# Optimization experiments

Measured on AMD Instinct MI355X. Metric: run time of the kernel, lower is better.

Reference implementation:

```python
import jax, jax.numpy as jnp
import numpy as np

N_NODES, BATCH, VOCAB, HID, OUT = 2047, 128, 32, 128, 128


def setup_inputs() -> dict:
    key = jax.random.key(0)
    ks = jax.random.split(key, 18)
    w = 0.05  # small init scale (xavier-ish for these sizes)
    rn = lambda k, s, sc=w: jax.random.normal(k, s, dtype=jnp.float32) * sc
    return {
        "targets": jax.random.normal(ks[0], (N_NODES, BATCH, VOCAB), dtype=jnp.float32),
        "masks": jnp.ones((N_NODES, BATCH), dtype=jnp.float32),
        "wir_w": rn(ks[1], (HID, VOCAB)), "wir_b": rn(ks[2], (HID,)),
        "whr_w": rn(ks[3], (HID, 2 * HID)), "whr_b": rn(ks[4], (HID,)),
        "wiz_w": rn(ks[5], (HID, VOCAB)), "wiz_b": rn(ks[6], (HID,)),
        "whz_w": rn(ks[7], (HID, 2 * HID)), "whz_b": rn(ks[8], (HID,)),
        "win_w": rn(ks[9], (HID, VOCAB)), "win_b": rn(ks[10], (HID,)),
        "whn_w": rn(ks[11], (HID, 2 * HID)), "whn_b": rn(ks[12], (HID,)),
        "mu_w": rn(ks[13], (OUT, HID)), "mu_b": rn(ks[14], (OUT,)),
        "lv_w": rn(ks[15], (OUT, HID)), "lv_b": rn(ks[16], (OUT,)),
    }


def _encode(targets, masks, wir_w, wir_b, whr_w, whr_b, wiz_w, wiz_b,
            whz_w, whz_b, win_w, win_b, whn_w, whn_b):
    # Complete binary tree in heap layout: level d occupies nodes [2^d-1, 2^(d+1)-1).
    # Bottom-up level sweep == the original node-by-node recursion, but each
    # level's GRU221 cells are batched into one fused GEMM group.
    Nn, B, V = targets.shape
    H = wir_w.shape[0]
    D = int(np.log2(Nn + 1))  # static at trace time
    h_prev = None  # hidden states of the level below, [2^(d+1)*B, H]
    for d in range(D - 1, -1, -1):
        n = 1 << d
        start = n - 1
        x = targets[start:start + n].reshape(n * B, V)
        m = masks[start:start + n].reshape(n * B, 1)
        if h_prev is None:  # leaves: zero children
            h1 = jnp.zeros((n * B, H), dtype=targets.dtype)
            h2 = h1
        else:
            hp = h_prev.reshape(2 * n, B, H)
            h1 = hp[0::2].reshape(n * B, H)  # left children (heap idx 2i+1)
            h2 = hp[1::2].reshape(n * B, H)  # right children (heap idx 2i+2)
        h = jnp.concatenate([h1, h2], axis=1)  # [nB, 2H]
        r = jax.nn.sigmoid(x @ wir_w.T + wir_b + h @ whr_w.T + whr_b)
        z = jax.nn.sigmoid(x @ wiz_w.T + wiz_b + h @ whz_w.T + whz_b)
        c = jnp.tanh(x @ win_w.T + win_b + r * (h @ whn_w.T + whn_b))
        h_out = (1 - z) * c + z * 0.5 * h1 + z * 0.5 * h2
        h_prev = h_out * m
    return h_prev  # root hidden, [B, H]


def reference(targets, masks, wir_w, wir_b, whr_w, whr_b, wiz_w, wiz_b,
              whz_w, whz_b, win_w, win_b, whn_w, whn_b,
              mu_w, mu_b, lv_w, lv_b):
    root = _encode(targets, masks, wir_w, wir_b, whr_w, whr_b,
                   wiz_w, wiz_b, whz_w, whz_b, win_w, win_b, whn_w, whn_b)
    mu = root @ mu_w.T + mu_b
    logvar = root @ lv_w.T + lv_b
    return mu, logvar
```

## Files before the change

kernel.cpp:

```cpp
#include <hip/hip_runtime.h>
#include <hip/hip_bf16.h>
#include <math.h>

#define B 128
#define V 32
#define H 128
#define LDH 264
#define NT 512

typedef __attribute__((ext_vector_type(8))) short bf16x8;
typedef __attribute__((ext_vector_type(4))) float f32x4;

__device__ inline f32x4 mfma_wx(bf16x8 wf, bf16x8 xf, f32x4 c) {
    return __builtin_amdgcn_mfma_f32_16x16x32_bf16(wf, xf, c, 0, 0, 0);
}
__device__ inline unsigned short f2bf(float f) {
    __hip_bfloat16 h = __float2bfloat16(f);
    return __builtin_bit_cast(unsigned short, h);
}
__device__ inline float bf2f(unsigned short u) {
    unsigned int x = ((unsigned int)u) << 16;
    return __builtin_bit_cast(float, x);
}
__device__ inline float sig_pre(float y)  { return __builtin_amdgcn_rcpf(1.f + __builtin_amdgcn_exp2f(y)); }
__device__ inline float tanh_pre(float y) { return 1.f - 2.f * __builtin_amdgcn_rcpf(__builtin_amdgcn_exp2f(y) + 1.f); }
__device__ inline bf16x8 load_xfrag(const float* p) {
    float4 a = *(const float4*)p;
    float4 b = *(const float4*)(p + 4);
    bf16x8 r;
    r[0] = (short)f2bf(a.x); r[1] = (short)f2bf(a.y);
    r[2] = (short)f2bf(a.z); r[3] = (short)f2bf(a.w);
    r[4] = (short)f2bf(b.x); r[5] = (short)f2bf(b.y);
    r[6] = (short)f2bf(b.z); r[7] = (short)f2bf(b.w);
    return r;
}
__device__ inline uint2 pack4(float a, float b, float c, float d) {
    uint2 r;
    r.x = (unsigned int)f2bf(a) | ((unsigned int)f2bf(b) << 16);
    r.y = (unsigned int)f2bf(c) | ((unsigned int)f2bf(d) << 16);
    return r;
}

__global__ void prep_pack(const float* __restrict__ wir_w, const float* __restrict__ whr_w,
                          const float* __restrict__ wiz_w, const float* __restrict__ whz_w,
                          const float* __restrict__ win_w, const float* __restrict__ whn_w,
                          const float* __restrict__ wir_b, const float* __restrict__ whr_b,
                          const float* __restrict__ wiz_b, const float* __restrict__ whz_b,
                          const float* __restrict__ win_b, const float* __restrict__ whn_b,
                          const float* __restrict__ mu_w, const float* __restrict__ mu_b,
                          const float* __restrict__ lv_w, const float* __restrict__ lv_b,
                          unsigned short* __restrict__ wFrag, unsigned short* __restrict__ pFrag,
                          float* __restrict__ bias)
{
    int idx = blockIdx.x * blockDim.x + threadIdx.x;
    if (idx < 13824) {
        int lane = idx & 63;
        int ctks = idx >> 6;
        int ct = ctks % 24;
        int ks = ctks / 24;
        int g = ct >> 3;
        int t = ct & 7;
        int u = t * 16 + (lane & 15);
        const float scl = (g == 2) ? 2.88539008f : -1.44269504f;
        const float* wi = (g == 0) ? wir_w : (g == 1) ? wiz_w : win_w;
        const float* wh = (g == 0) ? whr_w : (g == 1) ? whz_w : whn_w;
        unsigned short v[8] __attribute__((aligned(16)));
        #pragma unroll
        for (int i = 0; i < 8; ++i) {
            float f;
            if (ks == 0) { int k = 8 * (lane >> 4) + i; f = wi[u * V + k]; }
            else         { int k = (ks - 1) * 32 + 8 * (lane >> 4) + i; f = wh[u * 256 + k]; }
            v[i] = f2bf(f * scl);
        }
        *(int4*)(wFrag + (size_t)idx * 8) = *(const int4*)v;
    } else if (idx < 13824 + 4096) {
        int pidx = idx - 13824;
        int lane = pidx & 63;
        int rest = pidx >> 6;
        int ct2 = rest & 15;
        int ks = rest >> 4;
        int sel = ct2 >> 3, tl = ct2 & 7;
        int u = tl * 16 + (lane & 15);
        const float* wsrc = sel ? lv_w : mu_w;
        unsigned short v[8] __attribute__((aligned(16)));
        #pragma unroll
        for (int i = 0; i < 8; ++i) {
            int k = ks * 32 + 8 * (lane >> 4) + i;
            v[i] = f2bf(wsrc[u * H + k]);
        }
        *(int4*)(pFrag + (size_t)pidx * 8) = *(const int4*)v;
    }
    if (idx < 6 * H) {
        int s = idx / H, u = idx % H;
        float val;
        if (s == 0)      val = (wir_b[u] + whr_b[u]) * -1.44269504f;
        else if (s == 1) val = (wiz_b[u] + whz_b[u]) * -1.44269504f;
        else if (s == 2) val = win_b[u] * 2.88539008f;
        else if (s == 3) val = whn_b[u] * 2.88539008f;
        else if (s == 4) val = mu_b[u];
        else             val = lv_b[u];
        bias[idx] = val;
    }
}

template <typename EMIT>
__device__ __forceinline__ void gru32_body(
    const unsigned short* __restrict__ wFrag, const float* __restrict__ bias,
    bf16x8 x0, bf16x8 x1, float m0, float m1,
    const unsigned short* __restrict__ hin,
    int lane, int w, EMIT emit)
{
    const int l15 = lane & 15;
    const int lg = lane >> 4;
    const int u0 = w * 16 + lg * 4;

    f32x4 acc_r[2], acc_z[2], acc_i[2], acc_h[2];
    {
        f32x4 b0 = *(const f32x4*)(bias + u0);
        f32x4 b1 = *(const f32x4*)(bias + 128 + u0);
        f32x4 b2 = *(const f32x4*)(bias + 256 + u0);
        f32x4 b3 = *(const f32x4*)(bias + 384 + u0);
        acc_r[0] = b0; acc_r[1] = b0;
        acc_z[0] = b1; acc_z[1] = b1;
        acc_i[0] = b2; acc_i[1] = b2;
        acc_h[0] = b3; acc_h[1] = b3;
    }
    {
        bf16x8 wr_ = *(const bf16x8*)(wFrag + ((size_t)(w) * 64 + lane) * 8);
        bf16x8 wz_ = *(const bf16x8*)(wFrag + ((size_t)(8 + w) * 64 + lane) * 8);
        bf16x8 wn_ = *(const bf16x8*)(wFrag + ((size_t)(16 + w) * 64 + lane) * 8);
        acc_r[0] = mfma_wx(wr_, x0, acc_r[0]);
        acc_r[1] = mfma_wx(wr_, x1, acc_r[1]);
        acc_z[0] = mfma_wx(wz_, x0, acc_z[0]);
        acc_z[1] = mfma_wx(wz_, x1, acc_z[1]);
        acc_i[0] = mfma_wx(wn_, x0, acc_i[0]);
        acc_i[1] = mfma_wx(wn_, x1, acc_i[1]);
    }
    #pragma unroll 2
    for (int ks = 1; ks <= 8; ++ks) {
        bf16x8 a0 = *(const bf16x8*)(&hin[l15 * LDH + (ks - 1) * 32 + 8 * lg]);
        bf16x8 a1 = *(const bf16x8*)(&hin[(16 + l15) * LDH + (ks - 1) * 32 + 8 * lg]);
        size_t fb = (size_t)ks * 24 * 64;
        bf16x8 wr_ = *(const bf16x8*)(wFrag + (fb + (size_t)(w) * 64 + lane) * 8);
        bf16x8 wz_ = *(const bf16x8*)(wFrag + (fb + (size_t)(8 + w) * 64 + lane) * 8);
        bf16x8 wn_ = *(const bf16x8*)(wFrag + (fb + (size_t)(16 + w) * 64 + lane) * 8);
        acc_r[0] = mfma_wx(wr_, a0, acc_r[0]);
        acc_r[1] = mfma_wx(wr_, a1, acc_r[1]);
        acc_z[0] = mfma_wx(wz_, a0, acc_z[0]);
        acc_z[1] = mfma_wx(wz_, a1, acc_z[1]);
        acc_h[0] = mfma_wx(wn_, a0, acc_h[0]);
        acc_h[1] = mfma_wx(wn_, a1, acc_h[1]);
    }
    #pragma unroll
    for (int rt = 0; rt < 2; ++rt) {
        float m = rt ? m1 : m0;
        int hrow = rt * 16 + l15;
        ushort4 h1v = *(const ushort4*)(&hin[hrow * LDH + u0]);
        ushort4 h2v = *(const ushort4*)(&hin[hrow * LDH + 128 + u0]);
        const unsigned short* h1p = (const unsigned short*)&h1v;
        const unsigned short* h2p = (const unsigned short*)&h2v;
        float ho[4];
        #pragma unroll
        for (int reg = 0; reg < 4; ++reg) {
            float rg = sig_pre(acc_r[rt][reg]);
            float zg = sig_pre(acc_z[rt][reg]);
            float cg = tanh_pre(acc_i[rt][reg] + rg * acc_h[rt][reg]);
            float hm = 0.5f * bf2f(h1p[reg]) + 0.5f * bf2f(h2p[reg]);
            ho[reg] = (cg + zg * (hm - cg)) * m;
        }
        emit(rt, u0, pack4(ho[0], ho[1], ho[2], ho[3]));
    }
}

__device__ __forceinline__ void load_wreg(
    const unsigned short* __restrict__ wFrag, int lane, int w,
    bf16x8 (&wr)[9], bf16x8 (&wz)[9], bf16x8 (&wn)[9])
{
    #pragma unroll
    for (int ks = 0; ks < 9; ++ks) {
        size_t fb = (size_t)ks * 24 * 64;
        wr[ks] = *(const bf16x8*)(wFrag + (fb + (size_t)(w) * 64 + lane) * 8);
        wz[ks] = *(const bf16x8*)(wFrag + (fb + (size_t)(8 + w) * 64 + lane) * 8);
        wn[ks] = *(const bf16x8*)(wFrag + (fb + (size_t)(16 + w) * 64 + lane) * 8);
    }
}

template <typename EMIT>
__device__ __forceinline__ void gru32_ws(
    const bf16x8 (&wr)[9], const bf16x8 (&wz)[9], const bf16x8 (&wn)[9],
    const float* __restrict__ bias,
    bf16x8 x0, bf16x8 x1, float m0, float m1,
    const unsigned short* __restrict__ hin,
    int lane, int w, EMIT emit)
{
    const int l15 = lane & 15;
    const int lg = lane >> 4;
    const int u0 = w * 16 + lg * 4;

    f32x4 acc_r[2], acc_z[2], acc_i[2], acc_h[2];
    {
        f32x4 b0 = *(const f32x4*)(bias + u0);
        f32x4 b1 = *(const f32x4*)(bias + 128 + u0);
        f32x4 b2 = *(const f32x4*)(bias + 256 + u0);
        f32x4 b3 = *(const f32x4*)(bias + 384 + u0);
        acc_r[0] = b0; acc_r[1] = b0;
        acc_z[0] = b1; acc_z[1] = b1;
        acc_i[0] = b2; acc_i[1] = b2;
        acc_h[0] = b3; acc_h[1] = b3;
    }
    acc_r[0] = mfma_wx(wr[0], x0, acc_r[0]);
    acc_r[1] = mfma_wx(wr[0], x1, acc_r[1]);
    acc_z[0] = mfma_wx(wz[0], x0, acc_z[0]);
    acc_z[1] = mfma_wx(wz[0], x1, acc_z[1]);
    acc_i[0] = mfma_wx(wn[0], x0, acc_i[0]);
    acc_i[1] = mfma_wx(wn[0], x1, acc_i[1]);
    #pragma unroll
    for (int ks = 1; ks <= 8; ++ks) {
        bf16x8 a0 = *(const bf16x8*)(&hin[l15 * LDH + (ks - 1) * 32 + 8 * lg]);
        bf16x8 a1 = *(const bf16x8*)(&hin[(16 + l15) * LDH + (ks - 1) * 32 + 8 * lg]);
        acc_r[0] = mfma_wx(wr[ks], a0, acc_r[0]);
        acc_r[1] = mfma_wx(wr[ks], a1, acc_r[1]);
        acc_z[0] = mfma_wx(wz[ks], a0, acc_z[0]);
        acc_z[1] = mfma_wx(wz[ks], a1, acc_z[1]);
        acc_h[0] = mfma_wx(wn[ks], a0, acc_h[0]);
        acc_h[1] = mfma_wx(wn[ks], a1, acc_h[1]);
    }
    #pragma unroll
    for (int rt = 0; rt < 2; ++rt) {
        float m = rt ? m1 : m0;
        int hrow = rt * 16 + l15;
        ushort4 h1v = *(const ushort4*)(&hin[hrow * LDH + u0]);
        ushort4 h2v = *(const ushort4*)(&hin[hrow * LDH + 128 + u0]);
        const unsigned short* h1p = (const unsigned short*)&h1v;
        const unsigned short* h2p = (const unsigned short*)&h2v;
        float ho[4];
        #pragma unroll
        for (int reg = 0; reg < 4; ++reg) {
            float rg = sig_pre(acc_r[rt][reg]);
            float zg = sig_pre(acc_z[rt][reg]);
            float cg = tanh_pre(acc_i[rt][reg] + rg * acc_h[rt][reg]);
            float hm = 0.5f * bf2f(h1p[reg]) + 0.5f * bf2f(h2p[reg]);
            ho[reg] = (cg + zg * (hm - cg)) * m;
        }
        emit(rt, u0, pack4(ho[0], ho[1], ho[2], ho[3]));
    }
}

__global__ __launch_bounds__(NT, 4) void subtree8_kernel(
    const float* __restrict__ targets, const float* __restrict__ masks,
    unsigned short* __restrict__ lvl8,
    const unsigned short* __restrict__ wFrag, const float* __restrict__ bias)
{
    __shared__ __attribute__((aligned(16))) unsigned short h_lds[32 * LDH];
    __shared__ __attribute__((aligned(16))) unsigned short h2_lds[32 * LDH];

    const int tid = threadIdx.x;
    const int lane = tid & 63;
    const int w = tid >> 6;
    const int l15 = lane & 15;
    const int lg = lane >> 4;
    const int u0 = w * 16 + lg * 4;
    const int n = blockIdx.x >> 2;
    const int q = blockIdx.x & 3;

    for (int half = 0; half < 2; ++half) {
        const int j = 2 * n + half;
        const size_t r9 = (size_t)(511 + j) * B + (size_t)q * 32;

        #pragma unroll
        for (int c = 0; c < 2; ++c) {
            const size_t crow = (size_t)(1023 + 2 * j + c) * B + (size_t)q * 32;
            bf16x8 xf0 = load_xfrag(targets + (crow + l15) * V + 8 * lg);
            bf16x8 xf1 = load_xfrag(targets + (crow + 16 + l15) * V + 8 * lg);
            float m0 = masks[crow + l15];
            float m1 = masks[crow + 16 + l15];
            f32x4 ar[2], az[2], an[2], bh;
            {
                f32x4 b0 = *(const f32x4*)(bias + u0);
                f32x4 b1 = *(const f32x4*)(bias + 128 + u0);
                f32x4 b2 = *(const f32x4*)(bias + 256 + u0);
                bh       = *(const f32x4*)(bias + 384 + u0);
                ar[0] = b0; ar[1] = b0;
                az[0] = b1; az[1] = b1;
                an[0] = b2; an[1] = b2;
            }
            {
                bf16x8 wr_ = *(const bf16x8*)(wFrag + ((size_t)(w) * 64 + lane) * 8);
                bf16x8 wz_ = *(const bf16x8*)(wFrag + ((size_t)(8 + w) * 64 + lane) * 8);
                bf16x8 wn_ = *(const bf16x8*)(wFrag + ((size_t)(16 + w) * 64 + lane) * 8);
                ar[0] = mfma_wx(wr_, xf0, ar[0]);
                ar[1] = mfma_wx(wr_, xf1, ar[1]);
                az[0] = mfma_wx(wz_, xf0, az[0]);
                az[1] = mfma_wx(wz_, xf1, az[1]);
                an[0] = mfma_wx(wn_, xf0, an[0]);
                an[1] = mfma_wx(wn_, xf1, an[1]);
            }
            #pragma unroll
            for (int rt = 0; rt < 2; ++rt) {
                float m = rt ? m1 : m0;
                int row = rt * 16 + l15;
                float ho[4];
                #pragma unroll
                for (int reg = 0; reg < 4; ++reg) {
                    float rg = sig_pre(ar[rt][reg]);
                    float zg = sig_pre(az[rt][reg]);
                    float cg = tanh_pre(an[rt][reg] + rg * bh[reg]);
                    ho[reg] = (cg - zg * cg) * m;
                }
                *(uint2*)(&h_lds[row * LDH + c * 128 + u0]) = pack4(ho[0], ho[1], ho[2], ho[3]);
            }
        }
        __syncthreads();

        {
            bf16x8 x9_0 = load_xfrag(targets + (r9 + l15) * V + 8 * lg);
            bf16x8 x9_1 = load_xfrag(targets + (r9 + 16 + l15) * V + 8 * lg);
            float m0 = masks[r9 + l15];
            float m1 = masks[r9 + 16 + l15];
            gru32_body(wFrag, bias, x9_0, x9_1, m0, m1, h_lds, lane, w,
                [&](int rt, int uu, uint2 pk) {
                    int row = rt * 16 + l15;
                    *(uint2*)(&h2_lds[row * LDH + half * 128 + uu]) = pk;
                });
        }
        __syncthreads();
    }

    {
        const size_t r8 = (size_t)(255 + n) * B + (size_t)q * 32;
        bf16x8 x8_0 = load_xfrag(targets + (r8 + l15) * V + 8 * lg);
        bf16x8 x8_1 = load_xfrag(targets + (r8 + 16 + l15) * V + 8 * lg);
        float m0 = masks[r8 + l15];
        float m1 = masks[r8 + 16 + l15];
        gru32_body(wFrag, bias, x8_0, x8_1, m0, m1, h2_lds, lane, w,
            [&](int rt, int uu, uint2 pk) {
                int row = rt * 16 + l15;
                *(uint2*)(lvl8 + ((size_t)n * B + (size_t)q * 32 + row) * H + uu) = pk;
            });
    }
}

__global__ __launch_bounds__(NT, 2) void tail4_kernel(
    const float* __restrict__ targets, const float* __restrict__ masks,
    const unsigned short* __restrict__ prev,
    unsigned short* __restrict__ outg,
    int s3, int s2, int s1, int s0,
    const unsigned short* __restrict__ wFrag, const float* __restrict__ bias,
    int do_proj, const unsigned short* __restrict__ pFrag, float* __restrict__ proj_out)
{
    __shared__ __attribute__((aligned(16))) unsigned short hc[32 * LDH];
    __shared__ __attribute__((aligned(16))) unsigned short h6[2 * 32 * LDH];
    __shared__ __attribute__((aligned(16))) unsigned short h5[32 * LDH];
    __shared__ __attribute__((aligned(16))) unsigned short h4[16 * LDH];

    const int tid = threadIdx.x;
    const int lane = tid & 63;
    const int w = tid >> 6;
    const int l15 = lane & 15;
    const int lg = lane >> 4;
    const int u0 = w * 16 + lg * 4;
    const int pr = blockIdx.x >> 3;
    const int c8 = blockIdx.x & 7;

    bf16x8 wr[9], wz[9], wn[9];
    load_wreg(wFrag, lane, w, wr, wz, wn);

    for (int s = 0; s < 4; ++s) {
        const int l1 = 4 * pr + s;
        #pragma unroll
        for (int t = 0; t < 2; ++t) {
            int task = t * NT + tid;
            int row = task >> 5;
            int ck = task & 31;
            int g = 4 * l1 + 2 * (row >> 4) + (ck >> 4);
            int4 v = *(const int4*)(prev + (((size_t)g) * B + (size_t)c8 * 16 + (row & 15)) * H + (ck & 15) * 8);
            *(int4*)(&hc[row * LDH + ck * 8]) = v;
        }
        size_t xr0 = ((size_t)(s3 + 2 * l1)) * B + (size_t)c8 * 16 + l15;
        size_t xr1 = ((size_t)(s3 + 2 * l1 + 1)) * B + (size_t)c8 * 16 + l15;
        bf16x8 xc0 = load_xfrag(targets + xr0 * V + 8 * lg);
        bf16x8 xc1 = load_xfrag(targets + xr1 * V + 8 * lg);
        float m0 = masks[xr0];
        float m1 = masks[xr1];
        __syncthreads();
        unsigned short* hout = h6 + (size_t)(s >> 1) * 32 * LDH;
        int rowbase = 16 * (s & 1);
        gru32_ws(wr, wz, wn, bias, xc0, xc1, m0, m1, hc, lane, w,
            [&](int rt, int uu, uint2 pk) {
                *(uint2*)(&hout[(rowbase + l15) * LDH + rt * 128 + uu]) = pk;
            });
        __syncthreads();
    }

    for (int k = 0; k < 2; ++k) {
        int n1 = 4 * pr + 2 * k;
        size_t xr0 = ((size_t)(s2 + n1)) * B + (size_t)c8 * 16 + l15;
        size_t xr1 = ((size_t)(s2 + n1 + 1)) * B + (size_t)c8 * 16 + l15;
        bf16x8 xc0 = load_xfrag(targets + xr0 * V + 8 * lg);
        bf16x8 xc1 = load_xfrag(targets + xr1 * V + 8 * lg);
        float m0 = masks[xr0];
        float m1 = masks[xr1];
        const unsigned short* hin = h6 + (size_t)k * 32 * LDH;
        int rowbase = 16 * k;
        gru32_ws(wr, wz, wn, bias, xc0, xc1, m0, m1, hin, lane, w,
            [&](int rt, int uu, uint2 pk) {
                *(uint2*)(&h5[(rowbase + l15) * LDH + rt * 128 + uu]) = pk;
            });
    }
    __syncthreads();

    {
        size_t xr0 = ((size_t)(s1 + 2 * pr)) * B + (size_t)c8 * 16 + l15;
        size_t xr1 = ((size_t)(s1 + 2 * pr + 1)) * B + (size_t)c8 * 16 + l15;
        bf16x8 xc0 = load_xfrag(targets + xr0 * V + 8 * lg);
        bf16x8 xc1 = load_xfrag(targets + xr1 * V + 8 * lg);
        float m0 = masks[xr0];
        float m1 = masks[xr1];
        gru32_ws(wr, wz, wn, bias, xc0, xc1, m0, m1, h5, lane, w,
            [&](int rt, int uu, uint2 pk) {
                *(uint2*)(&h4[l15 * LDH + rt * 128 + uu]) = pk;
            });
    }
    __syncthreads();

    {
        size_t xrp = ((size_t)(s0 + pr)) * B + (size_t)c8 * 16 + l15;
        bf16x8 xp = load_xfrag(targets + xrp * V + 8 * lg);
        float m = masks[xrp];
        f32x4 acc_r = *(const f32x4*)(bias + u0);
        f32x4 acc_z = *(const f32x4*)(bias + 128 + u0);
        f32x4 acc_i = *(const f32x4*)(bias + 256 + u0);
        f32x4 acc_h = *(const f32x4*)(bias + 384 + u0);
        acc_r = mfma_wx(wr[0], xp, acc_r);
        acc_z = mfma_wx(wz[0], xp, acc_z);
        acc_i = mfma_wx(wn[0], xp, acc_i);
        #pragma unroll
        for (int ks = 1; ks <= 8; ++ks) {
            bf16x8 a = *(const bf16x8*)(&h4[l15 * LDH + (ks - 1) * 32 + 8 * lg]);
            acc_r = mfma_wx(wr[ks], a, acc_r);
            acc_z = mfma_wx(wz[ks], a, acc_z);
            acc_h = mfma_wx(wn[ks], a, acc_h);
        }
        ushort4 h1v = *(const ushort4*)(&h4[l15 * LDH + u0]);
        ushort4 h2v = *(const ushort4*)(&h4[l15 * LDH + 128 + u0]);
        const unsigned short* h1p = (const unsigned short*)&h1v;
        const unsigned short* h2p = (const unsigned short*)&h2v;
        float ho[4];
        #pragma unroll
        for (int reg = 0; reg < 4; ++reg) {
            float rg = sig_pre(acc_r[reg]);
            float zg = sig_pre(acc_z[reg]);
            float cg = tanh_pre(acc_i[reg] + rg * acc_h[reg]);
            float hm = 0.5f * bf2f(h1p[reg]) + 0.5f * bf2f(h2p[reg]);
            ho[reg] = (cg + zg * (hm - cg)) * m;
        }
        uint2 pk = pack4(ho[0], ho[1], ho[2], ho[3]);
        if (outg)
            *(uint2*)(outg + ((size_t)pr * B + (size_t)c8 * 16 + l15) * H + u0) = pk;
        if (do_proj)
            *(uint2*)(&hc[l15 * LDH + u0]) = pk;
    }

    if (do_proj) {
        __syncthreads();
        f32x4 pa[2];
        #pragma unroll
        for (int jj = 0; jj < 2; ++jj) {
            int ct2 = 2 * w + jj;
            int sel = ct2 >> 3, tl = ct2 & 7;
            pa[jj] = *(const f32x4*)(bias + 512 + sel * 128 + tl * 16 + lg * 4);
        }
        #pragma unroll
        for (int ks = 0; ks < 4; ++ks) {
            bf16x8 a = *(const bf16x8*)(&hc[l15 * LDH + ks * 32 + 8 * lg]);
            #pragma unroll
            for (int jj = 0; jj < 2; ++jj) {
                bf16x8 f = *(const bf16x8*)(pFrag + (((size_t)ks * 16 + 2 * w + jj) * 64 + lane) * 8);
                pa[jj] = mfma_wx(f, a, pa[jj]);
            }
        }
        #pragma unroll
        for (int jj = 0; jj < 2; ++jj) {
            int ct2 = 2 * w + jj;
            int sel = ct2 >> 3, tl = ct2 & 7;
            int up = tl * 16 + lg * 4;
            int row = c8 * 16 + l15;
            *(f32x4*)(proj_out + ((size_t)sel * B + row) * H + up) = pa[jj];
        }
    }
}

extern "C" void kernel_launch(void* const* d_in, const int* in_sizes, int n_in,
                              void* d_out, int out_size, void* d_ws, size_t ws_size,
                              hipStream_t stream)
{
    const float* targets = (const float*)d_in[0];
    const float* masks   = (const float*)d_in[1];
    const float* wir_w = (const float*)d_in[2];  const float* wir_b = (const float*)d_in[3];
    const float* whr_w = (const float*)d_in[4];  const float* whr_b = (const float*)d_in[5];
    const float* wiz_w = (const float*)d_in[6];  const float* wiz_b = (const float*)d_in[7];
    const float* whz_w = (const float*)d_in[8];  const float* whz_b = (const float*)d_in[9];
    const float* win_w = (const float*)d_in[10]; const float* win_b = (const float*)d_in[11];
    const float* whn_w = (const float*)d_in[12]; const float* whn_b = (const float*)d_in[13];
    const float* mu_w  = (const float*)d_in[14]; const float* mu_b  = (const float*)d_in[15];
    const float* lv_w  = (const float*)d_in[16]; const float* lv_b  = (const float*)d_in[17];

    unsigned short* ws16 = (unsigned short*)d_ws;
    unsigned short* lvl8 = ws16;
    unsigned short* lvl4 = lvl8 + (size_t)256 * B * H;
    unsigned short* wFrag = lvl4 + (size_t)16 * B * H;
    unsigned short* pFrag = wFrag + 110592;
    float*          biasw = (float*)(pFrag + 32768);

    prep_pack<<<70, 256, 0, stream>>>(
        wir_w, whr_w, wiz_w, whz_w, win_w, whn_w,
        wir_b, whr_b, wiz_b, whz_b, win_b, whn_b,
        mu_w, mu_b, lv_w, lv_b, wFrag, pFrag, biasw);

    subtree8_kernel<<<1024, NT, 0, stream>>>(targets, masks, lvl8, wFrag, biasw);

    tail4_kernel<<<128, NT, 0, stream>>>(
        targets, masks, lvl8, lvl4, 127, 63, 31, 15,
        wFrag, biasw, 0, nullptr, nullptr);

    tail4_kernel<<<8, NT, 0, stream>>>(
        targets, masks, lvl4, nullptr, 7, 3, 1, 0,
        wFrag, biasw, 1, pFrag, (float*)d_out);
}
```

Baseline: 110.2 us.

## Prefetch next-stage inputs and double-buffer child states to overlap loads with compute

In subtree8_kernel the loop over the two halves is unrolled by hand, and the global loads of targets for the second half and for level 8 are issued before the barrier and the compute of the prior stage. In tail4_kernel the staging buffer for child hidden states is double-buffered (hcA/hcB), so the next step's child states and targets are fetched from global memory while the current GRU step runs. This is meant to hide global load latency behind MFMA work and drop one barrier per step. In exchange it raises register pressure, and tail4's launch bounds drop to one block per SM to make room, which may cost occupancy.

```diff
diff --git a/kernel.cpp b/kernel.cpp
--- a/kernel.cpp
+++ b/kernel.cpp
@@ -24,15 +24,19 @@
 }
 __device__ inline float sig_pre(float y)  { return __builtin_amdgcn_rcpf(1.f + __builtin_amdgcn_exp2f(y)); }
 __device__ inline float tanh_pre(float y) { return 1.f - 2.f * __builtin_amdgcn_rcpf(__builtin_amdgcn_exp2f(y) + 1.f); }
-__device__ inline bf16x8 load_xfrag(const float* p) {
-    float4 a = *(const float4*)p;
-    float4 b = *(const float4*)(p + 4);
+
+__device__ inline bf16x8 cvt_xfrag(float4 a, float4 b) {
     bf16x8 r;
     r[0] = (short)f2bf(a.x); r[1] = (short)f2bf(a.y);
     r[2] = (short)f2bf(a.z); r[3] = (short)f2bf(a.w);
     r[4] = (short)f2bf(b.x); r[5] = (short)f2bf(b.y);
     r[6] = (short)f2bf(b.z); r[7] = (short)f2bf(b.w);
     return r;
+}
+__device__ inline bf16x8 load_xfrag(const float* p) {
+    float4 a = *(const float4*)p;
+    float4 b = *(const float4*)(p + 4);
+    return cvt_xfrag(a, b);
 }
 __device__ inline uint2 pack4(float a, float b, float c, float d) {
     uint2 r;
@@ -100,6 +104,51 @@
         else if (s == 4) val = mu_b[u];
         else             val = lv_b[u];
         bias[idx] = val;
+    }
+}
+
+__device__ __forceinline__ void leaf_tile(
+    const unsigned short* __restrict__ wFrag, const float* __restrict__ bias,
+    bf16x8 xf0, bf16x8 xf1, float m0, float m1,
+    unsigned short* __restrict__ h_lds, int c, int lane, int w)
+{
+    const int l15 = lane & 15;
+    const int lg = lane >> 4;
+    const int u0 = w * 16 + lg * 4;
+    f32x4 ar[2], az[2], an[2], bh;
+    {
+        f32x4 b0 = *(const f32x4*)(bias + u0);
+        f32x4 b1 = *(const f32x4*)(bias + 128 + u0);
+        f32x4 b2 = *(const f32x4*)(bias + 256 + u0);
+        bh       = *(const f32x4*)(bias + 384 + u0);
+        ar[0] = b0; ar[1] = b0;
+        az[0] = b1; az[1] = b1;
+        an[0] = b2; an[1] = b2;
+    }
+    {
+        bf16x8 wr_ = *(const bf16x8*)(wFrag + ((size_t)(w) * 64 + lane) * 8);
+        bf16x8 wz_ = *(const bf16x8*)(wFrag + ((size_t)(8 + w) * 64 + lane) * 8);
+        bf16x8 wn_ = *(const bf16x8*)(wFrag + ((size_t)(16 + w) * 64 + lane) * 8);
+        ar[0] = mfma_wx(wr_, xf0, ar[0]);
+        ar[1] = mfma_wx(wr_, xf1, ar[1]);
+        az[0] = mfma_wx(wz_, xf0, az[0]);
+        az[1] = mfma_wx(wz_, xf1, az[1]);
+        an[0] = mfma_wx(wn_, xf0, an[0]);
+        an[1] = mfma_wx(wn_, xf1, an[1]);
+    }
+    #pragma unroll
+    for (int rt = 0; rt < 2; ++rt) {
+        float m = rt ? m1 : m0;
+        int row = rt * 16 + l15;
+        float ho[4];
+        #pragma unroll
+        for (int reg = 0; reg < 4; ++reg) {
+            float rg = sig_pre(ar[rt][reg]);
+            float zg = sig_pre(az[rt][reg]);
+            float cg = tanh_pre(an[rt][reg] + rg * bh[reg]);
+            ho[reg] = (cg - zg * cg) * m;
+        }
+        *(uint2*)(&h_lds[row * LDH + c * 128 + u0]) = pack4(ho[0], ho[1], ho[2], ho[3]);
     }
 }
 
@@ -259,80 +308,87 @@
     const int w = tid >> 6;
     const int l15 = lane & 15;
     const int lg = lane >> 4;
-    const int u0 = w * 16 + lg * 4;
     const int n = blockIdx.x >> 2;
     const int q = blockIdx.x & 3;
 
-    for (int half = 0; half < 2; ++half) {
-        const int j = 2 * n + half;
-        const size_t r9 = (size_t)(511 + j) * B + (size_t)q * 32;
-
-        #pragma unroll
-        for (int c = 0; c < 2; ++c) {
-            const size_t crow = (size_t)(1023 + 2 * j + c) * B + (size_t)q * 32;
-            bf16x8 xf0 = load_xfrag(targets + (crow + l15) * V + 8 * lg);
-            bf16x8 xf1 = load_xfrag(targets + (crow + 16 + l15) * V + 8 * lg);
-            float m0 = masks[crow + l15];
-            float m1 = masks[crow + 16 + l15];
-            f32x4 ar[2], az[2], an[2], bh;
-            {
-                f32x4 b0 = *(const f32x4*)(bias + u0);
-                f32x4 b1 = *(const f32x4*)(bias + 128 + u0);
-                f32x4 b2 = *(const f32x4*)(bias + 256 + u0);
-                bh       = *(const f32x4*)(bias + 384 + u0);
-                ar[0] = b0; ar[1] = b0;
-                az[0] = b1; az[1] = b1;
-                an[0] = b2; an[1] = b2;
-            }
-            {
-                bf16x8 wr_ = *(const bf16x8*)(wFrag + ((size_t)(w) * 64 + lane) * 8);
-                bf16x8 wz_ = *(const bf16x8*)(wFrag + ((size_t)(8 + w) * 64 + lane) * 8);
-                bf16x8 wn_ = *(const bf16x8*)(wFrag + ((size_t)(16 + w) * 64 + lane) * 8);
-                ar[0] = mfma_wx(wr_, xf0, ar[0]);
-                ar[1] = mfma_wx(wr_, xf1, ar[1]);
-                az[0] = mfma_wx(wz_, xf0, az[0]);
-                az[1] = mfma_wx(wz_, xf1, az[1]);
-                an[0] = mfma_wx(wn_, xf0, an[0]);
-                an[1] = mfma_wx(wn_, xf1, an[1]);
-            }
-            #pragma unroll
-            for (int rt = 0; rt < 2; ++rt) {
-                float m = rt ? m1 : m0;
+    const int j0 = 2 * n, j1 = 2 * n + 1;
+    const size_t r9_0 = (size_t)(511 + j0) * B + (size_t)q * 32;
+    const size_t r9_1 = (size_t)(511 + j1) * B + (size_t)q * 32;
+    const size_t c00 = (size_t)(1023 + 2 * j0) * B + (size_t)q * 32;
+    const size_t c01 = c00 + B;
+    const size_t c10 = (size_t)(1023 + 2 * j1) * B + (size_t)q * 32;
+    const size_t c11 = c10 + B;
+    const size_t r8 = (size_t)(255 + n) * B + (size_t)q * 32;
+
+    bf16x8 a_l0 = load_xfrag(targets + (c00 + l15) * V + 8 * lg);
+    bf16x8 a_l1 = load_xfrag(targets + (c00 + 16 + l15) * V + 8 * lg);
+    bf16x8 a_l2 = load_xfrag(targets + (c01 + l15) * V + 8 * lg);
+    bf16x8 a_l3 = load_xfrag(targets + (c01 + 16 + l15) * V + 8 * lg);
+    bf16x8 a_x0 = load_xfrag(targets + (r9_0 + l15) * V + 8 * lg);
+    bf16x8 a_x1 = load_xfrag(targets + (r9_0 + 16 + l15) * V + 8 * lg);
+
+    leaf_tile(wFrag, bias, a_l0, a_l1, masks[c00 + l15], masks[c00 + 16 + l15], h_lds, 0, lane, w);
+    leaf_tile(wFrag, bias, a_l2, a_l3, masks[c01 + l15], masks[c01 + 16 + l15], h_lds, 1, lane, w);
+
+    float4 br[12];
+    {
+        const float* p0 = targets + (c10 + l15) * V + 8 * lg;
+        const float* p1 = targets + (c10 + 16 + l15) * V + 8 * lg;
+        const float* p2 = targets + (c11 + l15) * V + 8 * lg;
+        const float* p3 = targets + (c11 + 16 + l15) * V + 8 * lg;
+        const float* p4 = targets + (r9_1 + l15) * V + 8 * lg;
+        const float* p5 = targets + (r9_1 + 16 + l15) * V + 8 * lg;
+        br[0] = *(const float4*)p0; br[1] = *(const float4*)(p0 + 4);
+        br[2] = *(const float4*)p1; br[3] = *(const float4*)(p1 + 4);
+        br[4] = *(const float4*)p2; br[5] = *(const float4*)(p2 + 4);
+        br[6] = *(const float4*)p3; br[7] = *(const float4*)(p3 + 4);
+        br[8] = *(const float4*)p4; br[9] = *(const float4*)(p4 + 4);
+        br[10] = *(const float4*)p5; br[11] = *(const float4*)(p5 + 4);
+    }
+    __syncthreads();
+
+    gru32_body(wFrag, bias, a_x0, a_x1, masks[r9_0 + l15], masks[r9_0 + 16 + l15],
+               h_lds, lane, w,
+        [&](int rt, int uu, uint2 pk) {
+            int row = rt * 16 + l15;
+            *(uint2*)(&h2_lds[row * LDH + uu]) = pk;
+        });
+    __syncthreads();
+
+    {
+        bf16x8 b_l0 = cvt_xfrag(br[0], br[1]);
+        bf16x8 b_l1 = cvt_xfrag(br[2], br[3]);
+        bf16x8 b_l2 = cvt_xfrag(br[4], br[5]);
+        bf16x8 b_l3 = cvt_xfrag(br[6], br[7]);
+        leaf_tile(wFrag, bias, b_l0, b_l1, masks[c10 + l15], masks[c10 + 16 + l15], h_lds, 0, lane, w);
+        leaf_tile(wFrag, bias, b_l2, b_l3, masks[c11 + l15], masks[c11 + 16 + l15], h_lds, 1, lane, w);
+    }
+    float4 dr[4];
+    {
+        const float* p0 = targets + (r8 + l15) * V + 8 * lg;
+        const float* p1 = targets + (r8 + 16 + l15) * V + 8 * lg;
+        dr[0] = *(const float4*)p0; dr[1] = *(const float4*)(p0 + 4);
+        dr[2] = *(const float4*)p1; dr[3] = *(const float4*)(p1 + 4);
+    }
+    __syncthreads();
+
+    {
+        bf16x8 b_x0 = cvt_xfrag(br[8], br[9]);
+        bf16x8 b_x1 = cvt_xfrag(br[10], br[11]);
+        gru32_body(wFrag, bias, b_x0, b_x1, masks[r9_1 + l15], masks[r9_1 + 16 + l15],
+                   h_lds, lane, w,
+            [&](int rt, int uu, uint2 pk) {
                 int row = rt * 16 + l15;
-                float ho[4];
-                #pragma unroll
-                for (int reg = 0; reg < 4; ++reg) {
-                    float rg = sig_pre(ar[rt][reg]);
-                    float zg = sig_pre(az[rt][reg]);
-                    float cg = tanh_pre(an[rt][reg] + rg * bh[reg]);
-                    ho[reg] = (cg - zg * cg) * m;
-                }
-                *(uint2*)(&h_lds[row * LDH + c * 128 + u0]) = pack4(ho[0], ho[1], ho[2], ho[3]);
-            }
-        }
-        __syncthreads();
-
-        {
-            bf16x8 x9_0 = load_xfrag(targets + (r9 + l15) * V + 8 * lg);
-            bf16x8 x9_1 = load_xfrag(targets + (r9 + 16 + l15) * V + 8 * lg);
-            float m0 = masks[r9 + l15];
-            float m1 = masks[r9 + 16 + l15];
-            gru32_body(wFrag, bias, x9_0, x9_1, m0, m1, h_lds, lane, w,
-                [&](int rt, int uu, uint2 pk) {
-                    int row = rt * 16 + l15;
-                    *(uint2*)(&h2_lds[row * LDH + half * 128 + uu]) = pk;
-                });
-        }
-        __syncthreads();
-    }
-
-    {
-        const size_t r8 = (size_t)(255 + n) * B + (size_t)q * 32;
-        bf16x8 x8_0 = load_xfrag(targets + (r8 + l15) * V + 8 * lg);
-        bf16x8 x8_1 = load_xfrag(targets + (r8 + 16 + l15) * V + 8 * lg);
-        float m0 = masks[r8 + l15];
-        float m1 = masks[r8 + 16 + l15];
-        gru32_body(wFrag, bias, x8_0, x8_1, m0, m1, h2_lds, lane, w,
+                *(uint2*)(&h2_lds[row * LDH + 128 + uu]) = pk;
+            });
+    }
+    __syncthreads();
+
+    {
+        bf16x8 d_x0 = cvt_xfrag(dr[0], dr[1]);
+        bf16x8 d_x1 = cvt_xfrag(dr[2], dr[3]);
+        gru32_body(wFrag, bias, d_x0, d_x1, masks[r8 + l15], masks[r8 + 16 + l15],
+                   h2_lds, lane, w,
             [&](int rt, int uu, uint2 pk) {
                 int row = rt * 16 + l15;
                 *(uint2*)(lvl8 + ((size_t)n * B + (size_t)q * 32 + row) * H + uu) = pk;
@@ -340,7 +396,7 @@
     }
 }
 
-__global__ __launch_bounds__(NT, 2) void tail4_kernel(
+__global__ __launch_bounds__(NT, 1) void tail4_kernel(
     const float* __restrict__ targets, const float* __restrict__ masks,
     const unsigned short* __restrict__ prev,
     unsigned short* __restrict__ outg,
@@ -348,7 +404,8 @@
     const unsigned short* __restrict__ wFrag, const float* __restrict__ bias,
     int do_proj, const unsigned short* __restrict__ pFrag, float* __restrict__ proj_out)
 {
-    __shared__ __attribute__((aligned(16))) unsigned short hc[32 * LDH];
+    __shared__ __attribute__((aligned(16))) unsigned short hcA[32 * LDH];
+    __shared__ __attribute__((aligned(16))) unsigned short hcB[32 * LDH];
     __shared__ __attribute__((aligned(16))) unsigned short h6[2 * 32 * LDH];
     __shared__ __attribute__((aligned(16))) unsigned short h5[32 * LDH];
     __shared__ __attribute__((aligned(16))) unsigned short h4[16 * LDH];
@@ -365,37 +422,62 @@
     bf16x8 wr[9], wz[9], wn[9];
     load_wreg(wFrag, lane, w, wr, wz, wn);
 
-    for (int s = 0; s < 4; ++s) {
-        const int l1 = 4 * pr + s;
-        #pragma unroll
-        for (int t = 0; t < 2; ++t) {
-            int task = t * NT + tid;
-            int row = task >> 5;
-            int ck = task & 31;
-            int g = 4 * l1 + 2 * (row >> 4) + (ck >> 4);
-            int4 v = *(const int4*)(prev + (((size_t)g) * B + (size_t)c8 * 16 + (row & 15)) * H + (ck & 15) * 8);
-            *(int4*)(&hc[row * LDH + ck * 8]) = v;
-        }
-        size_t xr0 = ((size_t)(s3 + 2 * l1)) * B + (size_t)c8 * 16 + l15;
-        size_t xr1 = ((size_t)(s3 + 2 * l1 + 1)) * B + (size_t)c8 * 16 + l15;
-        bf16x8 xc0 = load_xfrag(targets + xr0 * V + 8 * lg);
-        bf16x8 xc1 = load_xfrag(targets + xr1 * V + 8 * lg);
-        float m0 = masks[xr0];
-        float m1 = masks[xr1];
+    const int row0 = tid >> 5, ck0 = tid & 31;
+    const int row1 = (NT + tid) >> 5, ck1 = (NT + tid) & 31;
+    auto stage_src = [&](int l1v, int row, int ck) -> const unsigned short* {
+        int g = 4 * l1v + 2 * (row >> 4) + (ck >> 4);
+        return prev + (((size_t)g) * B + (size_t)c8 * 16 + (row & 15)) * H + (ck & 15) * 8;
+    };
+
+    {
+        int4 sv0 = *(const int4*)stage_src(4 * pr, row0, ck0);
+        int4 sv1 = *(const int4*)stage_src(4 * pr, row1, ck1);
+        *(int4*)(&hcA[row0 * LDH + ck0 * 8]) = sv0;
+        *(int4*)(&hcA[row1 * LDH + ck1 * 8]) = sv1;
+        size_t xr0 = ((size_t)(s3 + 8 * pr)) * B + (size_t)c8 * 16 + l15;
+        size_t xr1 = xr0 + B;
+        bf16x8 xp0 = load_xfrag(targets + xr0 * V + 8 * lg);
+        bf16x8 xp1 = load_xfrag(targets + xr1 * V + 8 * lg);
+        float pm0 = masks[xr0], pm1 = masks[xr1];
         __syncthreads();
-        unsigned short* hout = h6 + (size_t)(s >> 1) * 32 * LDH;
-        int rowbase = 16 * (s & 1);
-        gru32_ws(wr, wz, wn, bias, xc0, xc1, m0, m1, hc, lane, w,
-            [&](int rt, int uu, uint2 pk) {
-                *(uint2*)(&hout[(rowbase + l15) * LDH + rt * 128 + uu]) = pk;
-            });
-        __syncthreads();
+
+        for (int s = 0; s < 4; ++s) {
+            const unsigned short* cur = (s & 1) ? hcB : hcA;
+            unsigned short* nxt = (s & 1) ? hcA : hcB;
+            int4 nv0, nv1;
+            float4 xnr0, xnr1, xnr2, xnr3;
+            size_t nxr0 = 0, nxr1 = 0;
+            if (s < 3) {
+                nv0 = *(const int4*)stage_src(4 * pr + s + 1, row0, ck0);
+                nv1 = *(const int4*)stage_src(4 * pr + s + 1, row1, ck1);
+                nxr0 = ((size_t)(s3 + 2 * (4 * pr + s + 1))) * B + (size_t)c8 * 16 + l15;
+                nxr1 = nxr0 + B;
+                const float* p0 = targets + nxr0 * V + 8 * lg;
+                const float* p1 = targets + nxr1 * V + 8 * lg;
+                xnr0 = *(const float4*)p0; xnr1 = *(const float4*)(p0 + 4);
+                xnr2 = *(const float4*)p1; xnr3 = *(const float4*)(p1 + 4);
+            }
+            unsigned short* hout = h6 + (size_t)(s >> 1) * 32 * LDH;
+            int rowbase = 16 * (s & 1);
+            gru32_ws(wr, wz, wn, bias, xp0, xp1, pm0, pm1, cur, lane, w,
+                [&](int rt, int uu, uint2 pk) {
+                    *(uint2*)(&hout[(rowbase + l15) * LDH + rt * 128 + uu]) = pk;
+                });
+            if (s < 3) {
+                *(int4*)(&nxt[row0 * LDH + ck0 * 8]) = nv0;
+                *(int4*)(&nxt[row1 * LDH + ck1 * 8]) = nv1;
+                xp0 = cvt_xfrag(xnr0, xnr1);
+                xp1 = cvt_xfrag(xnr2, xnr3);
+                pm0 = masks[nxr0]; pm1 = masks[nxr1];
+            }
+            __syncthreads();
+        }
     }
 
     for (int k = 0; k < 2; ++k) {
         int n1 = 4 * pr + 2 * k;
         size_t xr0 = ((size_t)(s2 + n1)) * B + (size_t)c8 * 16 + l15;
-        size_t xr1 = ((size_t)(s2 + n1 + 1)) * B + (size_t)c8 * 16 + l15;
+        size_t xr1 = xr0 + B;
         bf16x8 xc0 = load_xfrag(targets + xr0 * V + 8 * lg);
         bf16x8 xc1 = load_xfrag(targets + xr1 * V + 8 * lg);
         float m0 = masks[xr0];
@@ -411,7 +493,7 @@
 
     {
         size_t xr0 = ((size_t)(s1 + 2 * pr)) * B + (size_t)c8 * 16 + l15;
-        size_t xr1 = ((size_t)(s1 + 2 * pr + 1)) * B + (size_t)c8 * 16 + l15;
+        size_t xr1 = xr0 + B;
         bf16x8 xc0 = load_xfrag(targets + xr0 * V + 8 * lg);
         bf16x8 xc1 = load_xfrag(targets + xr1 * V + 8 * lg);
         float m0 = masks[xr0];
@@ -458,7 +540,7 @@
         if (outg)
             *(uint2*)(outg + ((size_t)pr * B + (size_t)c8 * 16 + l15) * H + u0) = pk;
         if (do_proj)
-            *(uint2*)(&hc[l15 * LDH + u0]) = pk;
+            *(uint2*)(&hcA[l15 * LDH + u0]) = pk;
     }
 
     if (do_proj) {
@@ -472,7 +554,7 @@
         }
         #pragma unroll
         for (int ks = 0; ks < 4; ++ks) {
-            bf16x8 a = *(const bf16x8*)(&hc[l15 * LDH + ks * 32 + 8 * lg]);
+            bf16x8 a = *(const bf16x8*)(&hcA[l15 * LDH + ks * 32 + 8 * lg]);
             #pragma unroll
             for (int jj = 0; jj < 2; ++jj) {
                 bf16x8 f = *(const bf16x8*)(pFrag + (((size_t)ks * 16 + 2 * w + jj) * 64 + lane) * 8);
```

Measured after the change: 115.1 us. 1.04x slower.
